# Optimization experiments

Hardware: AMD Instinct MI355X
Metric: run time of the kernel (lower is better)

The kernel has to match this reference:

```python
import jax, jax.numpy as jnp
import numpy as np
import math

PHI = (1.0 + math.sqrt(5.0)) / 2.0
V, D, L, N, H = 50257, 128, 2, 512, 8
DH = D // H
B, S = 2, 256


def setup_inputs() -> dict:
    key = jax.random.key(0)
    ks = jax.random.split(key, 16)
    lim = 0.5 * math.sqrt(6.0 / (N + D))  # xavier_uniform gain=0.5 for Linear(N->D)
    return {
        "tokens": jax.random.randint(ks[0], (B, S), 0, V),
        "emb": (jax.random.normal(ks[1], (V, 2 * D)) * 0.02) * 0.5,
        "wq": jax.random.normal(ks[2], (L, H, DH)) * 0.02,
        "bq": jnp.zeros((L, H, DH)),
        "wk": jax.random.normal(ks[3], (L, H, DH)) * 0.02,
        "bk": jnp.zeros((L, H, DH)),
        "w_out": jax.random.normal(ks[4], (L, D)) * 0.02,
        "b_out": jnp.zeros((L, D)),
        "out_scale": jnp.ones((L, D)) * 0.5,
        "Wf": jax.random.normal(ks[5], (L, N, D)) * 0.02,
        "Bf": jnp.zeros((L, N, D)),
        "proj_real": jax.random.uniform(ks[6], (L, D, N), minval=-lim, maxval=lim),
        "proj_imag": jax.random.uniform(ks[7], (L, D, N), minval=-lim, maxval=lim),
        "attn_scale": jnp.ones((L,)),
        "res_scale": jnp.ones((L,)),
        "out_proj": jax.random.normal(ks[8], (V, D)) * 0.02,
    }


def reference(tokens, emb, wq, bq, wk, bk, w_out, b_out, out_scale, Wf, Bf,
              proj_real, proj_imag, attn_scale, res_scale, out_proj):
    dtype = emb.dtype
    wb = emb[tokens]                      # [B,S,2D] token -> (w, b) pairs
    w_e, b_e = wb[..., :D], wb[..., D:]
    t = jnp.arange(S, dtype=dtype)        # timestep per position

    # Recurrent Euler state evolution: theta = s/(1+|w|) + b + t*PHI ; s' = cos+sin
    def step(s, inp):
        w_t, b_t, tt = inp
        theta = s / (1.0 + jnp.abs(w_t)) + b_t + tt * PHI
        s_new = jnp.cos(theta) + jnp.sin(theta)
        return s_new, s_new

    _, states = jax.lax.scan(
        step, jnp.zeros((B, D), dtype),
        (jnp.moveaxis(w_e, 1, 0), jnp.moveaxis(b_e, 1, 0), t))
    states = jnp.moveaxis(states, 0, 1)   # [B,S,D] cached states

    causal = jnp.tril(jnp.ones((S, S), bool))  # cache includes current state
    t_phi = t * PHI
    scale = math.sqrt(2 * DH)

    x = states
    for l in range(L):
        # --- Euler attention ---
        xh = x.reshape(B, S, H, DH)
        th_q = xh / (1.0 + jnp.abs(wq[l])) + bq[l] + t_phi[None, :, None, None]
        q = jnp.concatenate([jnp.cos(th_q), jnp.sin(th_q)], axis=-1)  # [B,S,H,2DH]
        kh = states.reshape(B, S, H, DH)
        th_k = kh / (1.0 + jnp.abs(wk[l])) + bk[l]
        k = jnp.concatenate([jnp.cos(th_k), jnp.sin(th_k)], axis=-1)
        scores = jnp.einsum('bqhd,bkhd->bhqk', q, k) / scale
        scores = jnp.where(causal[None, None], scores, -jnp.inf)
        wts = jax.nn.softmax(scores, axis=-1)
        # each head attends over full-width cached states; heads are summed
        context = jnp.einsum('bhqk,bkd->bqd', wts, states)
        th_o = context / (1.0 + jnp.abs(w_out[l])) + b_out[l] + t_phi[None, :, None]
        attn_out = out_scale[l] * (jnp.cos(th_o) + jnp.sin(th_o))
        # --- Resonant FFN (per-neuron interference) ---
        th_f = x[:, :, None, :] / (1.0 + jnp.abs(Wf[l])) + Bf[l] + t[None, :, None, None]
        cos_sum = jnp.cos(th_f).sum(axis=-1)   # [B,S,N]
        sin_sum = jnp.sin(th_f).sum(axis=-1)
        res = cos_sum @ proj_real[l].T + sin_sum @ proj_imag[l].T
        res = jax.nn.silu(res)
        # additive fusion
        x = x + attn_scale[l] * attn_out + res_scale[l] * res

    logits = x @ out_proj.T                # [B,S,V]
    return logits
```

## Files before the change

kernel.cpp:

```cpp
#include <hip/hip_runtime.h>
#include <hip/hip_bf16.h>

using bf16x8 = __attribute__((ext_vector_type(8))) short;
using f32x4  = __attribute__((ext_vector_type(4))) float;

constexpr int cV  = 50257;
constexpr int cD  = 128;
constexpr int cN  = 512;
constexpr int cS  = 256;

#define PHI_F    1.6180339887498949f
#define INV2PI_F 0.15915494309189535f
#define SQRT2_F  1.4142135623730951f

__device__ __forceinline__ float fract1(float x) { return x - floorf(x); }

#if __has_builtin(__builtin_amdgcn_sinf)
__device__ __forceinline__ float sin_rev(float r) { return __builtin_amdgcn_sinf(r); }
__device__ __forceinline__ float cos_rev(float r) { return __builtin_amdgcn_cosf(r); }
#else
__device__ __forceinline__ float sin_rev(float r) { return __sinf(r * 6.2831853071795865f); }
__device__ __forceinline__ float cos_rev(float r) { return __cosf(r * 6.2831853071795865f); }
#endif

__device__ __forceinline__ unsigned short f2bf(float f) {
  unsigned u = __float_as_uint(f);
  unsigned r = (u + 0x7FFFu + ((u >> 16) & 1u)) >> 16;
  return (unsigned short)r;
}

__global__ void k_setup(const int* __restrict__ tokens, const float* __restrict__ emb,
                        float2* __restrict__ mc,
                        const float* __restrict__ pr, const float* __restrict__ pi,
                        float* __restrict__ pTR, float* __restrict__ pTI) {
  int blk = blockIdx.x;
  if (blk < 256) {
    int idx = blk * 256 + threadIdx.x;
    int t = idx & 255, s = idx >> 8;
    int b = t >> 7, d = t & 127;
    int tok = tokens[b * cS + s];
    float w  = emb[tok * (2 * cD) + d];
    float be = emb[tok * (2 * cD) + cD + d];
    float m2 = SQRT2_F * INV2PI_F / (1.f + fabsf(w));
    float c  = fmaf((float)s, PHI_F, be) * INV2PI_F + 0.125f;
    mc[idx] = make_float2(m2, c);
  } else {
    int idx = (blk - 256) * 256 + threadIdx.x;
    int l = idx >> 16, rem = idx & 65535;
    int n = rem >> 7, d = rem & 127;
    int src = (l * cD + d) * cN + n;
    pTR[idx] = pr[src];
    pTI[idx] = pi[src];
  }
}

__global__ void k_scan(const float2* __restrict__ mc, float* __restrict__ states) {
  int t = threadIdx.x;
  int b = t >> 7, d = t & 127;
  float2 buf[8];
#pragma unroll
  for (int i = 0; i < 8; ++i) buf[i] = mc[i * 256 + t];
  float sv = 0.f;
  float* out = states + (b * cS) * cD + d;
#pragma unroll 8
  for (int s = 0; s < cS; ++s) {
    float2 v = buf[s & 7];
    if (s + 8 < cS) buf[s & 7] = mc[(s + 8) * 256 + t];
    float r = fmaf(sv, v.x, v.y);
    sv = sin_rev(fract1(r));
    out[s * cD] = sv * SQRT2_F;
  }
}

__global__ __launch_bounds__(512) void k_layer(const float* __restrict__ x, const float* __restrict__ states,
                                               const float* __restrict__ wq, const float* __restrict__ bq,
                                               const float* __restrict__ wk, const float* __restrict__ bk,
                                               const float* __restrict__ Wf, const float* __restrict__ Bf,
                                               float* __restrict__ ctx, float* __restrict__ U, float* __restrict__ Vv) {
  int blk = blockIdx.x;
  if (blk < 256) {
    __shared__ __align__(16) float qrow[2][256];
    __shared__ float Psum[2][256];
    __shared__ float redm[2][4], reds[2][4];
    __shared__ float cred[2][256];
    __shared__ __align__(16) float rkl[128], bkl[128];
    int b = blk >> 7, qp = blk & 127;
    int sub = threadIdx.x >> 8;
    int t = threadIdx.x & 255;
    int q = qp * 2 + sub;
    if (threadIdx.x < 128) {
      int hd = threadIdx.x;
      rkl[hd] = INV2PI_F / (1.f + fabsf(wk[hd]));
      bkl[hd] = bk[hd] * INV2PI_F;
    }
    if (t < 128) {
      int hd = t;
      float rq = 1.f / (1.f + fabsf(wq[hd]));
      float thq = fmaf(x[(b * cS + q) * cD + hd], rq, fmaf((float)q, PHI_F, bq[hd])) * INV2PI_F;
      float fq = fract1(thq);
      qrow[sub][hd]       = cos_rev(fq);
      qrow[sub][128 + hd] = sin_rev(fq);
    }
    Psum[sub][t] = 0.f;
    __syncthreads();
    bool act = (t <= q);
    float sc[8];
    const float4* Sr = (const float4*)(states + (b * cS + t) * cD);
#pragma unroll
    for (int h = 0; h < 8; ++h) {
      float sacc = 0.f;
#pragma unroll
      for (int j = 0; j < 4; ++j) {
        float4 sv4 = Sr[h * 4 + j];
        int hd = h * 16 + j * 4;
        float sva[4] = { sv4.x, sv4.y, sv4.z, sv4.w };
#pragma unroll
        for (int c = 0; c < 4; ++c) {
          float f = fract1(fmaf(sva[c], rkl[hd + c], bkl[hd + c]));
          float ck = cos_rev(f), sk = sin_rev(f);
          sacc = fmaf(qrow[sub][hd + c], ck, fmaf(qrow[sub][128 + hd + c], sk, sacc));
        }
      }
      sc[h] = act ? sacc * 0.17677669529663689f : -3.0e38f;
    }
    int wid = t >> 6;
    for (int h = 0; h < 8; ++h) {
      float v = sc[h];
#pragma unroll
      for (int off = 32; off; off >>= 1) v = fmaxf(v, __shfl_xor(v, off, 64));
      if ((t & 63) == 0) redm[sub][wid] = v;
      __syncthreads();
      float m = fmaxf(fmaxf(redm[sub][0], redm[sub][1]), fmaxf(redm[sub][2], redm[sub][3]));
      float p = act ? __expf(sc[h] - m) : 0.f;
      float ps = p;
#pragma unroll
      for (int off = 32; off; off >>= 1) ps += __shfl_xor(ps, off, 64);
      if ((t & 63) == 0) reds[sub][wid] = ps;
      __syncthreads();
      float tot = reds[sub][0] + reds[sub][1] + reds[sub][2] + reds[sub][3];
      Psum[sub][t] += p / tot;
    }
    __syncthreads();
    int d = t & 127, half = t >> 7;
    float acc = 0.f;
    int k0 = half * 128;
    int kend = min(k0 + 128, q + 1);
    for (int kk = k0; kk < kend; ++kk)
      acc = fmaf(Psum[sub][kk], states[(b * cS + kk) * cD + d], acc);
    cred[sub][t] = acc;
    __syncthreads();
    if (half == 0) ctx[(b * cS + q) * cD + d] = cred[sub][t] + cred[sub][t + 128];
  } else {
    int fblk = blk - 256;
    int ns = fblk & 15, tg = fblk >> 4;
    constexpr int P = 130;
    __shared__ __align__(16) float finv[32 * P];
    __shared__ __align__(16) float fb[32 * P];
    __shared__ __align__(16) float xl[32 * 128];
    int t = threadIdx.x;
#pragma unroll
    for (int i = 0; i < 8; ++i) {
      int idx = t + i * 512;
      int rl = idx >> 7, d = idx & 127;
      int g = (ns * 32 + rl) * cD + d;
      finv[rl * P + d] = INV2PI_F / (1.f + fabsf(Wf[g]));
      fb[rl * P + d]   = Bf[g] * INV2PI_F;
      xl[idx] = x[(tg * 32 + rl) * cD + d];
    }
    __syncthreads();
    int nl = t & 31, tli = t >> 5;
#pragma unroll
    for (int p = 0; p < 2; ++p) {
      int tl = p * 16 + tli;
      int T = tg * 32 + tl;
      float srev = (float)(T & 255) * INV2PI_F;
      float uc = 0.f, us = 0.f;
      const float* fi  = finv + nl * P;
      const float* fbp = fb + nl * P;
      const float* xr  = xl + tl * 128;
#pragma unroll 4
      for (int d = 0; d < cD; d += 2) {
        float2 fiv = *(const float2*)(fi + d);
        float2 fbv = *(const float2*)(fbp + d);
        float2 xv  = *(const float2*)(xr + d);
        float f0 = fract1(fmaf(xv.x, fiv.x, fbv.x) + srev);
        float f1 = fract1(fmaf(xv.y, fiv.y, fbv.y) + srev);
        uc += cos_rev(f0);
        us += sin_rev(f0);
        uc += cos_rev(f1);
        us += sin_rev(f1);
      }
      U[T * cN + ns * 32 + nl]  = uc;
      Vv[T * cN + ns * 32 + nl] = us;
    }
  }
}

__global__ __launch_bounds__(256) void k_res(const float* __restrict__ U, const float* __restrict__ Vv,
                                             const float* __restrict__ pTR, const float* __restrict__ pTI,
                                             const float* __restrict__ ctx, const float* __restrict__ x,
                                             const float* __restrict__ w_out, const float* __restrict__ b_out,
                                             const float* __restrict__ out_scale,
                                             const float* __restrict__ attn_scale, const float* __restrict__ res_scale,
                                             int l, float* __restrict__ xout, unsigned short* __restrict__ xbf) {
  int blk = blockIdx.x;
  int t = threadIdx.x;
  __shared__ __align__(16) float uv[4][512][2];
  __shared__ __align__(16) float4 part[128];
#pragma unroll
  for (int i = 0; i < 8; ++i) {
    int idx = t + i * 256;
    int tok = idx >> 9, n = idx & 511;
    uv[tok][n][0] = U[(blk * 4 + tok) * cN + n];
    uv[tok][n][1] = Vv[(blk * 4 + tok) * cN + n];
  }
  __syncthreads();
  int d4 = t & 31, g = t >> 5, tok = g & 3, nh = g >> 2;
  int T = blk * 4 + tok, s = T & 255;
  float a0 = 0.f, a1 = 0.f, a2 = 0.f, a3 = 0.f;
  const float* prB = pTR + (size_t)(l * cN) * cD + d4 * 4;
  const float* piB = pTI + (size_t)(l * cN) * cD + d4 * 4;
  int nEnd = nh * 256 + 256;
  for (int n = nh * 256; n < nEnd; ++n) {
    float4 pr = *(const float4*)(prB + n * cD);
    float4 pi = *(const float4*)(piB + n * cD);
    float2 w = *(const float2*)&uv[tok][n][0];
    a0 = fmaf(w.x, pr.x, fmaf(w.y, pi.x, a0));
    a1 = fmaf(w.x, pr.y, fmaf(w.y, pi.y, a1));
    a2 = fmaf(w.x, pr.z, fmaf(w.y, pi.z, a2));
    a3 = fmaf(w.x, pr.w, fmaf(w.y, pi.w, a3));
  }
  if (nh == 1) part[tok * 32 + d4] = make_float4(a0, a1, a2, a3);
  __syncthreads();
  if (nh == 0) {
    float4 p2 = part[tok * 32 + d4];
    float rr[4] = { a0 + p2.x, a1 + p2.y, a2 + p2.z, a3 + p2.w };
    int di = d4 * 4;
    float4 cx  = *(const float4*)(ctx + T * cD + di);
    float4 wo  = *(const float4*)(w_out + l * cD + di);
    float4 bo  = *(const float4*)(b_out + l * cD + di);
    float4 osc = *(const float4*)(out_scale + l * cD + di);
    float4 xv  = *(const float4*)(x + T * cD + di);
    float as = attn_scale[l], rs = res_scale[l];
    float sphi = (float)s * PHI_F;
    float cxa[4] = { cx.x, cx.y, cx.z, cx.w };
    float woa[4] = { wo.x, wo.y, wo.z, wo.w };
    float boa[4] = { bo.x, bo.y, bo.z, bo.w };
    float osa[4] = { osc.x, osc.y, osc.z, osc.w };
    float xva[4] = { xv.x, xv.y, xv.z, xv.w };
    float oa[4];
#pragma unroll
    for (int c = 0; c < 4; ++c) {
      float th = fmaf(cxa[c], 1.f / (1.f + fabsf(woa[c])), boa[c]) + sphi;
      float f = fract1(th * INV2PI_F);
      float ao = osa[c] * (cos_rev(f) + sin_rev(f));
      float r = rr[c];
      float sil = r / (1.f + __expf(-r));
      oa[c] = fmaf(as, ao, fmaf(rs, sil, xva[c]));
    }
    *(float4*)(xout + T * cD + di) = make_float4(oa[0], oa[1], oa[2], oa[3]);
    if (xbf) {
      ushort4 b4 = { f2bf(oa[0]), f2bf(oa[1]), f2bf(oa[2]), f2bf(oa[3]) };
      *(ushort4*)(xbf + T * cD + di) = b4;
    }
  }
}

__global__ __launch_bounds__(256) void k_gemm(const unsigned short* __restrict__ Xbf,
                                              const float* __restrict__ W,
                                              float* __restrict__ out) {
  __shared__ __align__(16) unsigned short Wl[64 * 128];
  __shared__ __align__(16) float Cw[4][16 * 64];
  int t = threadIdx.x;
  int v0 = blockIdx.x * 64;
#pragma unroll
  for (int i = 0; i < 8; ++i) {
    int idx = t + i * 256;
    int row = idx >> 5, c4 = idx & 31;
    int v = v0 + row;
    float4 wv = make_float4(0.f, 0.f, 0.f, 0.f);
    if (v < cV) wv = *(const float4*)(W + (size_t)v * cD + c4 * 4);
    ushort4 b4 = { f2bf(wv.x), f2bf(wv.y), f2bf(wv.z), f2bf(wv.w) };
    int byte = (row * 256 + c4 * 8) ^ ((row & 7) << 4);
    *(ushort4*)((char*)Wl + byte) = b4;
  }
  int wid = t >> 6, lane = t & 63;
  int lr = lane & 15, lk = lane >> 4;
  f32x4 acc[8][4];
#pragma unroll
  for (int fm = 0; fm < 8; ++fm)
#pragma unroll
    for (int fv = 0; fv < 4; ++fv) acc[fm][fv] = (f32x4){0.f, 0.f, 0.f, 0.f};
  __syncthreads();
#pragma unroll
  for (int ks = 0; ks < 4; ++ks) {
    bf16x8 a[8];
#pragma unroll
    for (int fm = 0; fm < 8; ++fm) {
      int row = wid * 128 + fm * 16 + lr;
      a[fm] = *(const bf16x8*)(Xbf + row * cD + ks * 32 + lk * 8);
    }
    bf16x8 bfr[4];
#pragma unroll
    for (int fv = 0; fv < 4; ++fv) {
      int v = fv * 16 + lr;
      int byte = (v * 256 + ks * 64 + lk * 16) ^ ((v & 7) << 4);
      bfr[fv] = *(const bf16x8*)((const char*)Wl + byte);
    }
#pragma unroll
    for (int fm = 0; fm < 8; ++fm)
#pragma unroll
      for (int fv = 0; fv < 4; ++fv)
        acc[fm][fv] = __builtin_amdgcn_mfma_f32_16x16x32_bf16(a[fm], bfr[fv], acc[fm][fv], 0, 0, 0);
  }
  bool full = (v0 + 64 <= cV);
  float* Cp = Cw[wid];
#pragma unroll
  for (int fm = 0; fm < 8; ++fm) {
#pragma unroll
    for (int fv = 0; fv < 4; ++fv) {
#pragma unroll
      for (int r = 0; r < 4; ++r) {
        int rowl = lk * 4 + r;
        int colw = fv * 16 + lr;
        Cp[(rowl * 64 + colw) ^ (((rowl >> 2) & 1) << 4)] = acc[fm][fv][r];
      }
    }
    int grow0 = wid * 128 + fm * 16;
#pragma unroll
    for (int r2 = 0; r2 < 4; ++r2) {
      int rowl = r2 * 4 + lk;
      float4 cv = *(const float4*)&Cp[(rowl * 64 + lr * 4) ^ ((r2 & 1) << 4)];
      int grow = grow0 + rowl;
      if (full) {
        *(float4*)(out + (size_t)grow * cV + v0 + lr * 4) = cv;
      } else {
        int cbase = v0 + lr * 4;
        float ca[4] = { cv.x, cv.y, cv.z, cv.w };
#pragma unroll
        for (int j = 0; j < 4; ++j)
          if (cbase + j < cV) out[(size_t)grow * cV + cbase + j] = ca[j];
      }
    }
  }
}

extern "C" void kernel_launch(void* const* d_in, const int* in_sizes, int n_in,
                              void* d_out, int out_size, void* d_ws, size_t ws_size,
                              hipStream_t stream) {
  const int*   tokens    = (const int*)d_in[0];
  const float* emb       = (const float*)d_in[1];
  const float* wq        = (const float*)d_in[2];
  const float* bq        = (const float*)d_in[3];
  const float* wk        = (const float*)d_in[4];
  const float* bk        = (const float*)d_in[5];
  const float* w_out     = (const float*)d_in[6];
  const float* b_out     = (const float*)d_in[7];
  const float* out_scale = (const float*)d_in[8];
  const float* Wf        = (const float*)d_in[9];
  const float* Bf        = (const float*)d_in[10];
  const float* pr        = (const float*)d_in[11];
  const float* pi        = (const float*)d_in[12];
  const float* attn_s    = (const float*)d_in[13];
  const float* res_s     = (const float*)d_in[14];
  const float* out_proj  = (const float*)d_in[15];
  float* out = (float*)d_out;
  float* ws  = (float*)d_ws;

  float*  states = ws;
  float*  x1     = ws + 65536;
  float*  x2     = ws + 131072;
  float*  ctx    = ws + 196608;
  float2* mc     = (float2*)(ws + 262144);
  float*  U      = ws + 393216;
  float*  Vv     = ws + 655360;
  float*  pTR    = ws + 917504;
  float*  pTI    = ws + 1048576;
  unsigned short* X2bf = (unsigned short*)(ws + 1179648);

  k_setup<<<768, 256, 0, stream>>>(tokens, emb, mc, pr, pi, pTR, pTI);
  k_scan<<<1, 256, 0, stream>>>(mc, states);

  const float* xin = states;
  float* xouts[2] = { x1, x2 };
  for (int l = 0; l < 2; ++l) {
    k_layer<<<512, 512, 0, stream>>>(xin, states, wq + l * 128, bq + l * 128,
                                     wk + l * 128, bk + l * 128,
                                     Wf + l * 65536, Bf + l * 65536, ctx, U, Vv);
    k_res<<<128, 256, 0, stream>>>(U, Vv, pTR, pTI, ctx, xin, w_out, b_out, out_scale,
                                   attn_s, res_s, l, xouts[l],
                                   (l == 1) ? X2bf : (unsigned short*)nullptr);
    xin = xouts[l];
  }
  k_gemm<<<(cV + 63) / 64, 256, 0, stream>>>(X2bf, out_proj, out);
}
```

Before: 188.8 us.

## Pre-convert out_proj to bf16 in setup, restructure GEMM and widen k_res grid

The fp32-to-bf16 conversion of out_proj moves out of the GEMM into the setup kernel, which writes a padded bf16 copy to workspace. The GEMM now reads bf16 fragments directly from global memory without LDS staging, splits the M dimension across two blocks, and prefetches A fragments for the next k-step. k_res switches from 4 tokens per block to one token per block with an 8-way n-split reduction, giving 512 blocks instead of 128. The cost is an extra pass over out_proj in setup (read fp32, write bf16) plus more redundant global reads of W fragments per block.

```diff
diff --git a/kernel.cpp b/kernel.cpp
--- a/kernel.cpp
+++ b/kernel.cpp
@@ -5,6 +5,7 @@
 using f32x4  = __attribute__((ext_vector_type(4))) float;
 
 constexpr int cV  = 50257;
+constexpr int cVp = 50304;
 constexpr int cD  = 128;
 constexpr int cN  = 512;
 constexpr int cS  = 256;
@@ -32,7 +33,8 @@
 __global__ void k_setup(const int* __restrict__ tokens, const float* __restrict__ emb,
                         float2* __restrict__ mc,
                         const float* __restrict__ pr, const float* __restrict__ pi,
-                        float* __restrict__ pTR, float* __restrict__ pTI) {
+                        float* __restrict__ pTR, float* __restrict__ pTI,
+                        const float* __restrict__ W, unsigned short* __restrict__ Wbf) {
   int blk = blockIdx.x;
   if (blk < 256) {
     int idx = blk * 256 + threadIdx.x;
@@ -44,13 +46,26 @@
     float m2 = SQRT2_F * INV2PI_F / (1.f + fabsf(w));
     float c  = fmaf((float)s, PHI_F, be) * INV2PI_F + 0.125f;
     mc[idx] = make_float2(m2, c);
-  } else {
+  } else if (blk < 768) {
     int idx = (blk - 256) * 256 + threadIdx.x;
     int l = idx >> 16, rem = idx & 65535;
     int n = rem >> 7, d = rem & 127;
     int src = (l * cD + d) * cN + n;
     pTR[idx] = pr[src];
     pTI[idx] = pi[src];
+  } else {
+    int idx = (blk - 768) * 256 + threadIdx.x;
+    int row = idx >> 4, c0 = (idx & 15) * 8;
+    ushort4 o0 = {0,0,0,0}, o1 = {0,0,0,0};
+    if (row < cV) {
+      float4 w0 = *(const float4*)(W + (size_t)row * cD + c0);
+      float4 w1 = *(const float4*)(W + (size_t)row * cD + c0 + 4);
+      o0 = { f2bf(w0.x), f2bf(w0.y), f2bf(w0.z), f2bf(w0.w) };
+      o1 = { f2bf(w1.x), f2bf(w1.y), f2bf(w1.z), f2bf(w1.w) };
+    }
+    unsigned short* dst = Wbf + (size_t)row * cD + c0;
+    *(ushort4*)dst = o0;
+    *(ushort4*)(dst + 4) = o1;
   }
 }
 
@@ -203,38 +218,40 @@
                                              const float* __restrict__ out_scale,
                                              const float* __restrict__ attn_scale, const float* __restrict__ res_scale,
                                              int l, float* __restrict__ xout, unsigned short* __restrict__ xbf) {
-  int blk = blockIdx.x;
+  int T = blockIdx.x;
   int t = threadIdx.x;
-  __shared__ __align__(16) float uv[4][512][2];
-  __shared__ __align__(16) float4 part[128];
-#pragma unroll
-  for (int i = 0; i < 8; ++i) {
-    int idx = t + i * 256;
-    int tok = idx >> 9, n = idx & 511;
-    uv[tok][n][0] = U[(blk * 4 + tok) * cN + n];
-    uv[tok][n][1] = Vv[(blk * 4 + tok) * cN + n];
-  }
+  __shared__ __align__(16) float uvU[512], uvV[512];
+  __shared__ __align__(16) float4 part[8][32];
+  uvU[t]       = U[T * cN + t];
+  uvU[t + 256] = U[T * cN + 256 + t];
+  uvV[t]       = Vv[T * cN + t];
+  uvV[t + 256] = Vv[T * cN + 256 + t];
   __syncthreads();
-  int d4 = t & 31, g = t >> 5, tok = g & 3, nh = g >> 2;
-  int T = blk * 4 + tok, s = T & 255;
+  int d4 = t & 31, nh = t >> 5;
   float a0 = 0.f, a1 = 0.f, a2 = 0.f, a3 = 0.f;
   const float* prB = pTR + (size_t)(l * cN) * cD + d4 * 4;
   const float* piB = pTI + (size_t)(l * cN) * cD + d4 * 4;
-  int nEnd = nh * 256 + 256;
-  for (int n = nh * 256; n < nEnd; ++n) {
+  int n0 = nh * 64;
+#pragma unroll 4
+  for (int n = n0; n < n0 + 64; ++n) {
     float4 pr = *(const float4*)(prB + n * cD);
     float4 pi = *(const float4*)(piB + n * cD);
-    float2 w = *(const float2*)&uv[tok][n][0];
-    a0 = fmaf(w.x, pr.x, fmaf(w.y, pi.x, a0));
-    a1 = fmaf(w.x, pr.y, fmaf(w.y, pi.y, a1));
-    a2 = fmaf(w.x, pr.z, fmaf(w.y, pi.z, a2));
-    a3 = fmaf(w.x, pr.w, fmaf(w.y, pi.w, a3));
-  }
-  if (nh == 1) part[tok * 32 + d4] = make_float4(a0, a1, a2, a3);
+    float wr = uvU[n], wi = uvV[n];
+    a0 = fmaf(wr, pr.x, fmaf(wi, pi.x, a0));
+    a1 = fmaf(wr, pr.y, fmaf(wi, pi.y, a1));
+    a2 = fmaf(wr, pr.z, fmaf(wi, pi.z, a2));
+    a3 = fmaf(wr, pr.w, fmaf(wi, pi.w, a3));
+  }
+  if (nh > 0) part[nh][d4] = make_float4(a0, a1, a2, a3);
   __syncthreads();
   if (nh == 0) {
-    float4 p2 = part[tok * 32 + d4];
-    float rr[4] = { a0 + p2.x, a1 + p2.y, a2 + p2.z, a3 + p2.w };
+    float rr[4] = { a0, a1, a2, a3 };
+#pragma unroll
+    for (int j = 1; j < 8; ++j) {
+      float4 p = part[j][d4];
+      rr[0] += p.x; rr[1] += p.y; rr[2] += p.z; rr[3] += p.w;
+    }
+    int s = T & 255;
     int di = d4 * 4;
     float4 cx  = *(const float4*)(ctx + T * cD + di);
     float4 wo  = *(const float4*)(w_out + l * cD + di);
@@ -266,80 +283,70 @@
   }
 }
 
-__global__ __launch_bounds__(256) void k_gemm(const unsigned short* __restrict__ Xbf,
-                                              const float* __restrict__ W,
-                                              float* __restrict__ out) {
-  __shared__ __align__(16) unsigned short Wl[64 * 128];
-  __shared__ __align__(16) float Cw[4][16 * 64];
-  int t = threadIdx.x;
-  int v0 = blockIdx.x * 64;
-#pragma unroll
-  for (int i = 0; i < 8; ++i) {
-    int idx = t + i * 256;
-    int row = idx >> 5, c4 = idx & 31;
-    int v = v0 + row;
-    float4 wv = make_float4(0.f, 0.f, 0.f, 0.f);
-    if (v < cV) wv = *(const float4*)(W + (size_t)v * cD + c4 * 4);
-    ushort4 b4 = { f2bf(wv.x), f2bf(wv.y), f2bf(wv.z), f2bf(wv.w) };
-    int byte = (row * 256 + c4 * 8) ^ ((row & 7) << 4);
-    *(ushort4*)((char*)Wl + byte) = b4;
-  }
-  int wid = t >> 6, lane = t & 63;
-  int lr = lane & 15, lk = lane >> 4;
-  f32x4 acc[8][4];
-#pragma unroll
-  for (int fm = 0; fm < 8; ++fm)
-#pragma unroll
-    for (int fv = 0; fv < 4; ++fv) acc[fm][fv] = (f32x4){0.f, 0.f, 0.f, 0.f};
-  __syncthreads();
+__global__ __launch_bounds__(512, 4) void k_gemm(const unsigned short* __restrict__ Xbf,
+                                                 const unsigned short* __restrict__ Wbf,
+                                                 float* __restrict__ out) {
+  __shared__ __align__(16) float Cw[8][16 * 36];
+  int t = threadIdx.x, bid = blockIdx.x;
+  int v0 = (bid >> 1) * 64, m0 = (bid & 1) * 256;
+  int wid = t >> 6, lane = t & 63, lr = lane & 15, lk = lane >> 4;
+  int wm = (wid >> 1) * 64, wv = (wid & 1) * 32;
+  const bf16x8* Xp = (const bf16x8*)Xbf;
+  const bf16x8* Wp = (const bf16x8*)Wbf;
+  bf16x8 b[4][2];
+#pragma unroll
+  for (int ks = 0; ks < 4; ++ks)
+#pragma unroll
+    for (int fv = 0; fv < 2; ++fv)
+      b[ks][fv] = Wp[(size_t)(v0 + wv + fv * 16 + lr) * 16 + ks * 4 + lk];
+  bf16x8 aCur[4], aNxt[4];
+#pragma unroll
+  for (int fm = 0; fm < 4; ++fm)
+    aCur[fm] = Xp[(m0 + wm + fm * 16 + lr) * 16 + lk];
+  f32x4 acc[4][2];
+#pragma unroll
+  for (int fm = 0; fm < 4; ++fm)
+#pragma unroll
+    for (int fv = 0; fv < 2; ++fv) acc[fm][fv] = (f32x4){0.f, 0.f, 0.f, 0.f};
 #pragma unroll
   for (int ks = 0; ks < 4; ++ks) {
-    bf16x8 a[8];
-#pragma unroll
-    for (int fm = 0; fm < 8; ++fm) {
-      int row = wid * 128 + fm * 16 + lr;
-      a[fm] = *(const bf16x8*)(Xbf + row * cD + ks * 32 + lk * 8);
-    }
-    bf16x8 bfr[4];
-#pragma unroll
-    for (int fv = 0; fv < 4; ++fv) {
-      int v = fv * 16 + lr;
-      int byte = (v * 256 + ks * 64 + lk * 16) ^ ((v & 7) << 4);
-      bfr[fv] = *(const bf16x8*)((const char*)Wl + byte);
-    }
-#pragma unroll
-    for (int fm = 0; fm < 8; ++fm)
-#pragma unroll
-      for (int fv = 0; fv < 4; ++fv)
-        acc[fm][fv] = __builtin_amdgcn_mfma_f32_16x16x32_bf16(a[fm], bfr[fv], acc[fm][fv], 0, 0, 0);
-  }
-  bool full = (v0 + 64 <= cV);
-  float* Cp = Cw[wid];
-#pragma unroll
-  for (int fm = 0; fm < 8; ++fm) {
-#pragma unroll
-    for (int fv = 0; fv < 4; ++fv) {
-#pragma unroll
-      for (int r = 0; r < 4; ++r) {
-        int rowl = lk * 4 + r;
-        int colw = fv * 16 + lr;
-        Cp[(rowl * 64 + colw) ^ (((rowl >> 2) & 1) << 4)] = acc[fm][fv][r];
-      }
-    }
-    int grow0 = wid * 128 + fm * 16;
-#pragma unroll
-    for (int r2 = 0; r2 < 4; ++r2) {
-      int rowl = r2 * 4 + lk;
-      float4 cv = *(const float4*)&Cp[(rowl * 64 + lr * 4) ^ ((r2 & 1) << 4)];
-      int grow = grow0 + rowl;
-      if (full) {
-        *(float4*)(out + (size_t)grow * cV + v0 + lr * 4) = cv;
-      } else {
-        int cbase = v0 + lr * 4;
-        float ca[4] = { cv.x, cv.y, cv.z, cv.w };
-#pragma unroll
-        for (int j = 0; j < 4; ++j)
-          if (cbase + j < cV) out[(size_t)grow * cV + cbase + j] = ca[j];
+    if (ks < 3) {
+#pragma unroll
+      for (int fm = 0; fm < 4; ++fm)
+        aNxt[fm] = Xp[(m0 + wm + fm * 16 + lr) * 16 + (ks + 1) * 4 + lk];
+    }
+#pragma unroll
+    for (int fm = 0; fm < 4; ++fm)
+#pragma unroll
+      for (int fv = 0; fv < 2; ++fv)
+        acc[fm][fv] = __builtin_amdgcn_mfma_f32_16x16x32_bf16(aCur[fm], b[ks][fv], acc[fm][fv], 0, 0, 0);
+#pragma unroll
+    for (int fm = 0; fm < 4; ++fm) aCur[fm] = aNxt[fm];
+  }
+  float* Cp = &Cw[wid][0];
+  int rowl = lane >> 2, cg = lane & 3;
+#pragma unroll
+  for (int fm = 0; fm < 4; ++fm) {
+#pragma unroll
+    for (int fv = 0; fv < 2; ++fv)
+#pragma unroll
+      for (int r = 0; r < 4; ++r)
+        Cp[(lk * 4 + r) * 36 + fv * 16 + lr] = acc[fm][fv][r];
+    float4 c0 = *(const float4*)&Cp[rowl * 36 + cg * 4];
+    float4 c1 = *(const float4*)&Cp[rowl * 36 + 16 + cg * 4];
+    size_t rb = (size_t)(m0 + wm + fm * 16 + rowl) * cV;
+    int cb0 = v0 + wv + cg * 4;
+    int cb1 = cb0 + 16;
+    if (cb1 + 3 < cV) {
+      *(float4*)(out + rb + cb0) = c0;
+      *(float4*)(out + rb + cb1) = c1;
+    } else {
+      float ca0[4] = { c0.x, c0.y, c0.z, c0.w };
+      float ca1[4] = { c1.x, c1.y, c1.z, c1.w };
+#pragma unroll
+      for (int j = 0; j < 4; ++j) {
+        if (cb0 + j < cV) out[rb + cb0 + j] = ca0[j];
+        if (cb1 + j < cV) out[rb + cb1 + j] = ca1[j];
       }
     }
   }
@@ -377,8 +384,10 @@
   float*  pTR    = ws + 917504;
   float*  pTI    = ws + 1048576;
   unsigned short* X2bf = (unsigned short*)(ws + 1179648);
-
-  k_setup<<<768, 256, 0, stream>>>(tokens, emb, mc, pr, pi, pTR, pTI);
+  unsigned short* Wbf  = (unsigned short*)(ws + 1212416);
+
+  k_setup<<<768 + (cVp * 16) / 256, 256, 0, stream>>>(tokens, emb, mc, pr, pi, pTR, pTI,
+                                                      out_proj, Wbf);
   k_scan<<<1, 256, 0, stream>>>(mc, states);
 
   const float* xin = states;
@@ -387,10 +396,10 @@
     k_layer<<<512, 512, 0, stream>>>(xin, states, wq + l * 128, bq + l * 128,
                                      wk + l * 128, bk + l * 128,
                                      Wf + l * 65536, Bf + l * 65536, ctx, U, Vv);
-    k_res<<<128, 256, 0, stream>>>(U, Vv, pTR, pTI, ctx, xin, w_out, b_out, out_scale,
+    k_res<<<512, 256, 0, stream>>>(U, Vv, pTR, pTI, ctx, xin, w_out, b_out, out_scale,
                                    attn_s, res_s, l, xouts[l],
                                    (l == 1) ? X2bf : (unsigned short*)nullptr);
     xin = xouts[l];
   }
-  k_gemm<<<(cV + 63) / 64, 256, 0, stream>>>(X2bf, out_proj, out);
-}
+  k_gemm<<<1572, 512, 0, stream>>>(X2bf, Wbf, out);
+}
```

New measurement: 179.7 us. 4.8% less time.
